# Kernel optimization log

Hardware: AMD Instinct MI355X
Metric: run time of the kernel (lower is better)

## Reference

```python
import jax, jax.numpy as jnp
import numpy as np

NUM_EMBEDDINGS = 8192
EMBEDDING_DIM = 32
L2_EPS = 1e-12  # matches torch F.normalize eps


def _l2_normalize(x, axis=-1):
    norm = jnp.linalg.norm(x, axis=axis, keepdims=True)
    return x / jnp.maximum(norm, L2_EPS)


def setup_inputs() -> dict:
    key = jax.random.key(0)
    k1, k2 = jax.random.split(key)
    inputs = jax.random.normal(k1, (32, 1024, EMBEDDING_DIM), dtype=jnp.float32)
    embeddings = jax.random.normal(k2, (NUM_EMBEDDINGS, EMBEDDING_DIM), dtype=jnp.float32)
    embeddings = _l2_normalize(embeddings, axis=1)  # buffer init: F.normalize(randn)
    return {"inputs": inputs, "embeddings": embeddings}


def reference(inputs, embeddings):
    input_shape = inputs.shape
    d = embeddings.shape[1]
    flat = inputs.reshape(-1, d)                      # [N, d]
    flat_n = _l2_normalize(flat, axis=1)              # F.normalize(flat, p=2, dim=1)
    # cosine similarity against codebook: [N, K]
    distances = jnp.einsum('nd,kd->nk', flat_n, embeddings)
    encoding_indices = jnp.argmax(distances, axis=1)  # [N]
    quantized = embeddings[encoding_indices].reshape(input_shape)
    # use_commitment=False branch: mse(quantized, inputs.detach())
    loss = jnp.mean((quantized - jax.lax.stop_gradient(inputs)) ** 2)
    # straight-through estimator
    quantized_st = inputs + jax.lax.stop_gradient(quantized - inputs)
    return quantized_st, loss, encoding_indices.reshape(input_shape[:-1])
```

## Files before the change

### kernel.cpp

```cpp
#include <hip/hip_runtime.h>

typedef short short8 __attribute__((ext_vector_type(8)));
typedef float f32x4 __attribute__((ext_vector_type(4)));

#define NROWS 32768
#define DIM 32
#define KCODES 8192
#define FLAG_CAP 4096
#define EPS_REL (1.0f/4096.0f)

#define WS_EHI  0
#define WS_ELO  (512*1024)
#define WS_IDX  (1024*1024)
#define WS_LIST (WS_IDX + 128*1024)
#define WS_CNT  (WS_LIST + FLAG_CAP*4)
#define WS_PART (WS_CNT + 64)

__device__ __forceinline__ unsigned short bf16_rne(float v){
    unsigned int u = __float_as_uint(v);
    unsigned int r = (u + 0x7fffu + ((u >> 16) & 1u)) >> 16;
    return (unsigned short)r;
}
__device__ __forceinline__ float bf16_to_f(unsigned short h){
    return __uint_as_float(((unsigned int)h) << 16);
}
__device__ __forceinline__ float dot4(const float4& a, const float4& b){
    return fmaf(a.w, b.w, fmaf(a.z, b.z, fmaf(a.y, b.y, a.x * b.x)));
}

__global__ __launch_bounds__(256) void vq_prep(
    const float* __restrict__ emb,
    unsigned short* __restrict__ ehi, unsigned short* __restrict__ elo,
    int* __restrict__ cnt)
{
    int r = blockIdx.x * 256 + threadIdx.x;
    if (r < 2) cnt[r] = 0;
    const float* er = emb + (size_t)r * DIM;
    short8* dh = (short8*)(ehi + (size_t)r * DIM);
    short8* dl = (short8*)(elo + (size_t)r * DIM);
    #pragma unroll
    for (int i = 0; i < 4; i++){
        float4 v0 = *(const float4*)(er + i*8);
        float4 v1 = *(const float4*)(er + i*8 + 4);
        float f[8] = {v0.x, v0.y, v0.z, v0.w, v1.x, v1.y, v1.z, v1.w};
        short8 a, b;
        #pragma unroll
        for (int j = 0; j < 8; j++){
            unsigned short h = bf16_rne(f[j]);
            a[j] = (short)h;
            b[j] = (short)bf16_rne(f[j] - bf16_to_f(h));
        }
        dh[i] = a; dl[i] = b;
    }
}

#define PROC(bh, bl, tcs)                                                        \
  {                                                                              \
    unsigned int tcv = (unsigned int)(tcs);                                      \
    _Pragma("unroll")                                                            \
    for (int rg = 0; rg < 4; ++rg){                                              \
      f32x4 acc = __builtin_amdgcn_mfma_f32_16x16x32_bf16(ahi[rg], bh, cbias[rg], 0, 0, 0); \
      acc = __builtin_amdgcn_mfma_f32_16x16x32_bf16(ahi[rg], bl, acc, 0, 0, 0);  \
      acc = __builtin_amdgcn_mfma_f32_16x16x32_bf16(alo[rg], bh, acc, 0, 0, 0);  \
      _Pragma("unroll")                                                          \
      for (int q = 0; q < 4; ++q){                                               \
        unsigned int u = (__float_as_uint(acc[q]) & maskv) | tcv;                \
        int rr = rg * 4 + q;                                                     \
        unsigned int nv2;                                                        \
        asm("v_med3_u32 %0, %1, %2, %3" : "=v"(nv2) : "v"(u), "v"(v1[rr]), "v"(v2[rr])); \
        v2[rr] = nv2;                                                            \
        v1[rr] = (u > v1[rr]) ? u : v1[rr];                                      \
      }                                                                          \
    }                                                                            \
  }

__global__ __launch_bounds__(512, 4) void vq_main_mfma(
    const float* __restrict__ inputs,
    const unsigned short* __restrict__ ehi,
    const unsigned short* __restrict__ elo,
    int* __restrict__ idxws, int* __restrict__ list, int* __restrict__ cnt)
{
    const int L = threadIdx.x & 63;
    const int w = threadIdx.x >> 6;
    const int rowbase = blockIdx.x * 64;

    __shared__ float snorm[64];
    __shared__ unsigned int sv1[8][64][17];
    __shared__ unsigned int sv2[8][64][17];
    __shared__ unsigned int pb1[8][64];
    __shared__ unsigned int pb2[8][64];
    __shared__ int          pbc[8][64];

    short8 ahi[4], alo[4];
    #pragma unroll
    for (int rg = 0; rg < 4; ++rg){
        const float* xr = inputs + (size_t)(rowbase + rg*16 + (L & 15)) * DIM + (L >> 4) * 8;
        float4 p0 = *(const float4*)xr;
        float4 p1 = *(const float4*)(xr + 4);
        float f[8] = {p0.x, p0.y, p0.z, p0.w, p1.x, p1.y, p1.z, p1.w};
        short8 h, l;
        #pragma unroll
        for (int i = 0; i < 8; i++){
            unsigned short hb = bf16_rne(f[i]);
            h[i] = (short)hb;
            l[i] = (short)bf16_rne(f[i] - bf16_to_f(hb));
        }
        ahi[rg] = h; alo[rg] = l;
        float s = dot4(p0, p0) + dot4(p1, p1);
        s += __shfl_xor(s, 16, 64);
        s += __shfl_xor(s, 32, 64);
        if (w == 0 && (L >> 4) == 0) snorm[rg*16 + L] = sqrtf(s);
    }
    __syncthreads();

    f32x4 cbias[4];
    #pragma unroll
    for (int rg = 0; rg < 4; ++rg){
        #pragma unroll
        for (int q = 0; q < 4; ++q)
            cbias[rg][q] = 2.0f * snorm[rg*16 + (L >> 4)*4 + q];
    }

    unsigned int maskv = 0xFFFFFFC0u;
    asm("" : "+v"(maskv));

    unsigned int v1[16], v2[16];
    #pragma unroll
    for (int r = 0; r < 16; r++){ v1[r] = 0u; v2[r] = 0u; }

    const unsigned short* ehp = ehi + (size_t)(w*1024 + (L & 15)) * DIM + (L >> 4) * 8;
    const unsigned short* elp = elo + (size_t)(w*1024 + (L & 15)) * DIM + (L >> 4) * 8;

    for (int t = 0; t < 64; t += 2){
        short8 bh0 = *(const short8*)(ehp);
        short8 bl0 = *(const short8*)(elp);
        short8 bh1 = *(const short8*)(ehp + 512);
        short8 bl1 = *(const short8*)(elp + 512);
        ehp += 1024; elp += 1024;
        PROC(bh0, bl0, 63 - t);
        PROC(bh1, bl1, 62 - t);
    }

    #pragma unroll
    for (int rg = 0; rg < 4; ++rg){
        #pragma unroll
        for (int q = 0; q < 4; ++q){
            int row = rg*16 + (L >> 4)*4 + q;
            sv1[w][row][L & 15] = v1[rg*4 + q];
            sv2[w][row][L & 15] = v2[rg*4 + q];
        }
    }
    __syncthreads();

    {
        int r = threadIdx.x & 63;
        int s = threadIdx.x >> 6;
        unsigned int b1 = 0u, b2 = 0u; int bc = 0;
        #pragma unroll
        for (int c = 0; c < 16; ++c){
            unsigned int u1 = sv1[s][r][c];
            unsigned int u2 = sv2[s][r][c];
            unsigned int mn = min(b1, u1);
            unsigned int mx = max(b2, u2);
            b2 = max(mn, mx);
            bool g = u1 > b1;
            b1 = g ? u1 : b1;
            bc = g ? c : bc;
        }
        pb1[s][r] = b1; pb2[s][r] = b2; pbc[s][r] = bc;
    }
    __syncthreads();

    if (threadIdx.x < 64){
        int r = threadIdx.x;
        unsigned int b1 = 0u, b2 = 0u; int bw = 0, bc = 0;
        #pragma unroll
        for (int s = 0; s < 8; ++s){
            unsigned int u1 = pb1[s][r];
            unsigned int u2 = pb2[s][r];
            unsigned int mn = min(b1, u1);
            unsigned int mx = max(b2, u2);
            b2 = max(mn, mx);
            bool g = u1 > b1;
            b1 = g ? u1 : b1;
            bw = g ? s : bw;
            bc = g ? pbc[s][r] : bc;
        }
        int t = 63 - (int)(b1 & 63u);
        int k = bw*1024 + t*16 + bc;
        int row = rowbase + r;
        idxws[row] = k;
        float f1 = __uint_as_float(b1 & 0xFFFFFFC0u);
        float f2 = __uint_as_float(b2 & 0xFFFFFFC0u);
        if (f1 - f2 <= snorm[r] * EPS_REL){
            int pos = atomicAdd(cnt, 1);
            if (pos < FLAG_CAP) list[pos] = row;
        }
    }
}

__global__ __launch_bounds__(256) void vq_refine(
    const float* __restrict__ inputs, const float* __restrict__ emb,
    int* __restrict__ idxws, const int* __restrict__ list, const int* __restrict__ cnt)
{
    int n = *cnt; if (n > FLAG_CAP) n = FLAG_CAP;
    __shared__ float sv[4]; __shared__ int si[4];
    for (int j = blockIdx.x; j < n; j += gridDim.x){
        int row = list[j];
        const float4* xr = (const float4*)(inputs + (size_t)row * DIM);
        float4 x0 = xr[0], x1 = xr[1], x2 = xr[2], x3 = xr[3];
        float4 x4 = xr[4], x5 = xr[5], x6 = xr[6], x7 = xr[7];
        float bv = -3.0e38f; int bi = 0x7fffffff;
        for (int c = threadIdx.x; c < KCODES; c += 256){
            const float4* ep = (const float4*)(emb + (size_t)c * DIM);
            float d = dot4(x0, ep[0]) + dot4(x1, ep[1]) + dot4(x2, ep[2]) + dot4(x3, ep[3])
                    + dot4(x4, ep[4]) + dot4(x5, ep[5]) + dot4(x6, ep[6]) + dot4(x7, ep[7]);
            if (d > bv || (d == bv && c < bi)){ bv = d; bi = c; }
        }
        #pragma unroll
        for (int off = 32; off; off >>= 1){
            float ov = __shfl_down(bv, off, 64);
            int   oi = __shfl_down(bi, off, 64);
            if (ov > bv || (ov == bv && oi < bi)){ bv = ov; bi = oi; }
        }
        if ((threadIdx.x & 63) == 0){ sv[threadIdx.x >> 6] = bv; si[threadIdx.x >> 6] = bi; }
        __syncthreads();
        if (threadIdx.x == 0){
            #pragma unroll
            for (int q = 1; q < 4; q++){
                if (sv[q] > bv || (sv[q] == bv && si[q] < bi)){ bv = sv[q]; bi = si[q]; }
            }
            idxws[row] = bi;
        }
        __syncthreads();
    }
}

__global__ __launch_bounds__(256) void vq_output(
    const float* __restrict__ inputs, const float* __restrict__ emb,
    const int* __restrict__ idxws,
    float* __restrict__ out_q, float* __restrict__ out_idx,
    float* __restrict__ part, int* __restrict__ ticket, float* __restrict__ out_loss)
{
    int row = blockIdx.x * 256 + threadIdx.x;
    int idx = idxws[row];
    const float4* ep = (const float4*)(emb + (size_t)idx * DIM);
    const float4* xr = (const float4*)(inputs + (size_t)row * DIM);
    float4* oq = (float4*)(out_q + (size_t)row * DIM);
    float s = 0.f;
    #pragma unroll
    for (int i = 0; i < 8; i++){
        float4 q = ep[i], x = xr[i];
        oq[i] = q;
        float dx = q.x - x.x, dy = q.y - x.y, dz = q.z - x.z, dw = q.w - x.w;
        s += dx*dx + dy*dy + dz*dz + dw*dw;
    }
    out_idx[row] = (float)idx;
    #pragma unroll
    for (int off = 32; off; off >>= 1) s += __shfl_down(s, off, 64);
    __shared__ float sp[4];
    __shared__ int tkt;
    if ((threadIdx.x & 63) == 0) sp[threadIdx.x >> 6] = s;
    __syncthreads();
    if (threadIdx.x == 0){
        part[blockIdx.x] = sp[0] + sp[1] + sp[2] + sp[3];
        __threadfence();
        tkt = atomicAdd(ticket, 1);
    }
    __syncthreads();
    if (tkt == (NROWS/256) - 1 && threadIdx.x < 64){
        __threadfence();
        float t = 0.f;
        for (int i = threadIdx.x; i < NROWS/256; i += 64) t += part[i];
        #pragma unroll
        for (int off = 32; off; off >>= 1) t += __shfl_down(t, off, 64);
        if (threadIdx.x == 0) *out_loss = t * (1.0f / ((float)NROWS * (float)DIM));
    }
}

extern "C" void kernel_launch(void* const* d_in, const int* in_sizes, int n_in,
                              void* d_out, int out_size, void* d_ws, size_t ws_size,
                              hipStream_t stream) {
    const float* inputs = (const float*)d_in[0];
    const float* emb    = (const float*)d_in[1];
    float* out      = (float*)d_out;
    float* out_q    = out;
    float* out_loss = out + (size_t)NROWS * DIM;
    float* out_idx  = out_loss + 1;

    char* ws = (char*)d_ws;
    unsigned short* ehi   = (unsigned short*)(ws + WS_EHI);
    unsigned short* elo   = (unsigned short*)(ws + WS_ELO);
    int*            idxws = (int*)(ws + WS_IDX);
    int*            list  = (int*)(ws + WS_LIST);
    int*            cnt   = (int*)(ws + WS_CNT);
    float*          part  = (float*)(ws + WS_PART);

    vq_prep     <<<dim3(KCODES/256), dim3(256), 0, stream>>>(emb, ehi, elo, cnt);
    vq_main_mfma<<<dim3(NROWS/64),   dim3(512), 0, stream>>>(inputs, ehi, elo, idxws, list, cnt);
    vq_refine   <<<dim3(256),        dim3(256), 0, stream>>>(inputs, emb, idxws, list, cnt);
    vq_output   <<<dim3(NROWS/256),  dim3(256), 0, stream>>>(inputs, emb, idxws, out_q, out_idx, part, cnt + 1, out_loss);
}
```

Measured before the change: 103.9 us.

## Split codebook across two blocks per row tile and fuse refine into output

The main MFMA kernel now launches twice as many blocks, each scanning half the codebook. Each block stages its top-2 candidates in the output buffer as scratch. The cross-lane reduction now uses wave shuffles and a ballot instead of a large shared-memory transpose. The separate refine kernel is removed: the output kernel merges the two halves, recomputes the input norm, flags near-ties and does the exact fp32 rescan per block before writing results. The intent is better occupancy and fewer launches and workspace round trips, at the risk of serialized per-block refine loops when many rows are flagged.

```diff
diff --git a/kernel.cpp b/kernel.cpp
--- a/kernel.cpp
+++ b/kernel.cpp
@@ -6,15 +6,12 @@
 #define NROWS 32768
 #define DIM 32
 #define KCODES 8192
-#define FLAG_CAP 4096
 #define EPS_REL (1.0f/4096.0f)
 
 #define WS_EHI  0
 #define WS_ELO  (512*1024)
-#define WS_IDX  (1024*1024)
-#define WS_LIST (WS_IDX + 128*1024)
-#define WS_CNT  (WS_LIST + FLAG_CAP*4)
-#define WS_PART (WS_CNT + 64)
+#define WS_PART (1024*1024)
+#define WS_CNT  (WS_PART + 4096)
 
 __device__ __forceinline__ unsigned short bf16_rne(float v){
     unsigned int u = __float_as_uint(v);
@@ -34,7 +31,7 @@
     int* __restrict__ cnt)
 {
     int r = blockIdx.x * 256 + threadIdx.x;
-    if (r < 2) cnt[r] = 0;
+    if (r == 0) cnt[0] = 0;
     const float* er = emb + (size_t)r * DIM;
     short8* dh = (short8*)(ehi + (size_t)r * DIM);
     short8* dl = (short8*)(elo + (size_t)r * DIM);
@@ -54,14 +51,14 @@
     }
 }
 
-#define PROC(bh, bl, tcs)                                                        \
+#define PROC(bhv, blv, tcs)                                                      \
   {                                                                              \
     unsigned int tcv = (unsigned int)(tcs);                                      \
     _Pragma("unroll")                                                            \
     for (int rg = 0; rg < 4; ++rg){                                              \
-      f32x4 acc = __builtin_amdgcn_mfma_f32_16x16x32_bf16(ahi[rg], bh, cbias[rg], 0, 0, 0); \
-      acc = __builtin_amdgcn_mfma_f32_16x16x32_bf16(ahi[rg], bl, acc, 0, 0, 0);  \
-      acc = __builtin_amdgcn_mfma_f32_16x16x32_bf16(alo[rg], bh, acc, 0, 0, 0);  \
+      f32x4 acc = __builtin_amdgcn_mfma_f32_16x16x32_bf16(ahi[rg], bhv, cbias[rg], 0, 0, 0); \
+      acc = __builtin_amdgcn_mfma_f32_16x16x32_bf16(ahi[rg], blv, acc, 0, 0, 0); \
+      acc = __builtin_amdgcn_mfma_f32_16x16x32_bf16(alo[rg], bhv, acc, 0, 0, 0); \
       _Pragma("unroll")                                                          \
       for (int q = 0; q < 4; ++q){                                               \
         unsigned int u = (__float_as_uint(acc[q]) & maskv) | tcv;                \
@@ -78,18 +75,18 @@
     const float* __restrict__ inputs,
     const unsigned short* __restrict__ ehi,
     const unsigned short* __restrict__ elo,
-    int* __restrict__ idxws, int* __restrict__ list, int* __restrict__ cnt)
+    unsigned int* __restrict__ qscr)
 {
     const int L = threadIdx.x & 63;
     const int w = threadIdx.x >> 6;
-    const int rowbase = blockIdx.x * 64;
+    const int rb    = blockIdx.x & 511;
+    const int half_ = blockIdx.x >> 9;
+    const int rowbase = rb * 64;
 
     __shared__ float snorm[64];
-    __shared__ unsigned int sv1[8][64][17];
-    __shared__ unsigned int sv2[8][64][17];
-    __shared__ unsigned int pb1[8][64];
-    __shared__ unsigned int pb2[8][64];
-    __shared__ int          pbc[8][64];
+    __shared__ unsigned int sv1[8][64];
+    __shared__ unsigned int sv2[8][64];
+    __shared__ int          scol[8][64];
 
     short8 ahi[4], alo[4];
     #pragma unroll
@@ -128,46 +125,53 @@
     #pragma unroll
     for (int r = 0; r < 16; r++){ v1[r] = 0u; v2[r] = 0u; }
 
-    const unsigned short* ehp = ehi + (size_t)(w*1024 + (L & 15)) * DIM + (L >> 4) * 8;
-    const unsigned short* elp = elo + (size_t)(w*1024 + (L & 15)) * DIM + (L >> 4) * 8;
-
-    for (int t = 0; t < 64; t += 2){
-        short8 bh0 = *(const short8*)(ehp);
-        short8 bl0 = *(const short8*)(elp);
-        short8 bh1 = *(const short8*)(ehp + 512);
-        short8 bl1 = *(const short8*)(elp + 512);
+    const int c0 = half_ * 4096 + w * 512;
+    const unsigned short* ehp = ehi + (size_t)(c0 + (L & 15)) * DIM + (L >> 4) * 8;
+    const unsigned short* elp = elo + (size_t)(c0 + (L & 15)) * DIM + (L >> 4) * 8;
+
+    for (int t = 0; t < 32; t += 2){
+        short8 b0h = *(const short8*)(ehp);
+        short8 b0l = *(const short8*)(elp);
+        short8 b1h = *(const short8*)(ehp + 512);
+        short8 b1l = *(const short8*)(elp + 512);
         ehp += 1024; elp += 1024;
-        PROC(bh0, bl0, 63 - t);
-        PROC(bh1, bl1, 62 - t);
-    }
-
-    #pragma unroll
-    for (int rg = 0; rg < 4; ++rg){
-        #pragma unroll
-        for (int q = 0; q < 4; ++q){
-            int row = rg*16 + (L >> 4)*4 + q;
-            sv1[w][row][L & 15] = v1[rg*4 + q];
-            sv2[w][row][L & 15] = v2[rg*4 + q];
-        }
-    }
-    __syncthreads();
-
-    {
-        int r = threadIdx.x & 63;
-        int s = threadIdx.x >> 6;
-        unsigned int b1 = 0u, b2 = 0u; int bc = 0;
-        #pragma unroll
-        for (int c = 0; c < 16; ++c){
-            unsigned int u1 = sv1[s][r][c];
-            unsigned int u2 = sv2[s][r][c];
-            unsigned int mn = min(b1, u1);
-            unsigned int mx = max(b2, u2);
-            b2 = max(mn, mx);
-            bool g = u1 > b1;
-            b1 = g ? u1 : b1;
-            bc = g ? c : bc;
-        }
-        pb1[s][r] = b1; pb2[s][r] = b2; pbc[s][r] = bc;
+        PROC(b0h, b0l, 31 - t);
+        PROC(b1h, b1l, 30 - t);
+    }
+
+    unsigned int p1[16];
+    #pragma unroll
+    for (int r = 0; r < 16; r++) p1[r] = v1[r];
+    #pragma unroll
+    for (int m = 1; m < 16; m <<= 1){
+        #pragma unroll
+        for (int r = 0; r < 16; r++){
+            unsigned int ov1 = __shfl_xor(v1[r], m, 64);
+            unsigned int ov2 = __shfl_xor(v2[r], m, 64);
+            unsigned int mn = min(v1[r], ov1);
+            v2[r] = max(max(v2[r], ov2), mn);
+            v1[r] = max(v1[r], ov1);
+        }
+    }
+    int colr[16];
+    #pragma unroll
+    for (int r = 0; r < 16; r++){
+        unsigned long long bm = __ballot(p1[r] == v1[r]);
+        unsigned int grp = (unsigned int)((bm >> ((L >> 4) << 4)) & 0xFFFFull);
+        colr[r] = __ffs(grp) - 1;
+    }
+
+    if ((L & 15) == 0){
+        #pragma unroll
+        for (int rg = 0; rg < 4; ++rg){
+            #pragma unroll
+            for (int q = 0; q < 4; ++q){
+                int row = rg*16 + (L >> 4)*4 + q;
+                sv1[w][row] = v1[rg*4 + q];
+                sv2[w][row] = v2[rg*4 + q];
+                scol[w][row] = colr[rg*4 + q];
+            }
+        }
     }
     __syncthreads();
 
@@ -176,45 +180,70 @@
         unsigned int b1 = 0u, b2 = 0u; int bw = 0, bc = 0;
         #pragma unroll
         for (int s = 0; s < 8; ++s){
-            unsigned int u1 = pb1[s][r];
-            unsigned int u2 = pb2[s][r];
+            unsigned int u1 = sv1[s][r];
+            unsigned int u2 = sv2[s][r];
             unsigned int mn = min(b1, u1);
-            unsigned int mx = max(b2, u2);
-            b2 = max(mn, mx);
+            b2 = max(max(b2, u2), mn);
             bool g = u1 > b1;
-            b1 = g ? u1 : b1;
-            bw = g ? s : bw;
-            bc = g ? pbc[s][r] : bc;
-        }
-        int t = 63 - (int)(b1 & 63u);
-        int k = bw*1024 + t*16 + bc;
+            if (g){ b1 = u1; bw = s; bc = scol[s][r]; }
+        }
+        int t = 31 - (int)(b1 & 63u);
+        int k = half_*4096 + bw*512 + t*16 + bc;
         int row = rowbase + r;
-        idxws[row] = k;
-        float f1 = __uint_as_float(b1 & 0xFFFFFFC0u);
-        float f2 = __uint_as_float(b2 & 0xFFFFFFC0u);
-        if (f1 - f2 <= snorm[r] * EPS_REL){
-            int pos = atomicAdd(cnt, 1);
-            if (pos < FLAG_CAP) list[pos] = row;
-        }
-    }
-}
-
-__global__ __launch_bounds__(256) void vq_refine(
+        unsigned int* qs = qscr + (size_t)row * 32 + half_ * 3;
+        qs[0] = b1; qs[1] = b2; qs[2] = (unsigned int)k;
+    }
+}
+
+__global__ __launch_bounds__(256) void vq_output(
     const float* __restrict__ inputs, const float* __restrict__ emb,
-    int* __restrict__ idxws, const int* __restrict__ list, const int* __restrict__ cnt)
+    float* __restrict__ out_q, float* __restrict__ out_idx,
+    float* __restrict__ part, int* __restrict__ ticket, float* __restrict__ out_loss)
 {
-    int n = *cnt; if (n > FLAG_CAP) n = FLAG_CAP;
+    const int row = blockIdx.x * 256 + threadIdx.x;
+    unsigned int* q32 = (unsigned int*)out_q;
+
+    unsigned int a1 = q32[(size_t)row*32 + 0];
+    unsigned int a2 = q32[(size_t)row*32 + 1];
+    unsigned int ak = q32[(size_t)row*32 + 2];
+    unsigned int b1 = q32[(size_t)row*32 + 3];
+    unsigned int b2 = q32[(size_t)row*32 + 4];
+    unsigned int bk = q32[(size_t)row*32 + 5];
+
+    unsigned int w1 = a1, wk = ak;
+    if (b1 > a1){ w1 = b1; wk = bk; }
+    unsigned int w2 = max(max(a2, b2), min(a1, b1));
+
+    const float4* xr = (const float4*)(inputs + (size_t)row * DIM);
+    float4 x0 = xr[0], x1 = xr[1], x2 = xr[2], x3 = xr[3];
+    float4 x4 = xr[4], x5 = xr[5], x6 = xr[6], x7 = xr[7];
+    float nrm = sqrtf(dot4(x0,x0)+dot4(x1,x1)+dot4(x2,x2)+dot4(x3,x3)
+                     +dot4(x4,x4)+dot4(x5,x5)+dot4(x6,x6)+dot4(x7,x7));
+
+    float f1 = __uint_as_float(w1 & 0xFFFFFFC0u);
+    float f2 = __uint_as_float(w2 & 0xFFFFFFC0u);
+    bool flag = (f1 - f2) <= nrm * EPS_REL;
+
+    __shared__ int frows[256];
+    __shared__ int corr[256];
+    __shared__ int fcnt;
+    if (threadIdx.x == 0) fcnt = 0;
+    corr[threadIdx.x] = -1;
+    __syncthreads();
+    if (flag){ int p = atomicAdd(&fcnt, 1); frows[p] = row; }
+    __syncthreads();
+
     __shared__ float sv[4]; __shared__ int si[4];
-    for (int j = blockIdx.x; j < n; j += gridDim.x){
-        int row = list[j];
-        const float4* xr = (const float4*)(inputs + (size_t)row * DIM);
-        float4 x0 = xr[0], x1 = xr[1], x2 = xr[2], x3 = xr[3];
-        float4 x4 = xr[4], x5 = xr[5], x6 = xr[6], x7 = xr[7];
+    for (int j = 0; j < fcnt; ++j){
+        int rr = frows[j];
+        const float4* yr = (const float4*)(inputs + (size_t)rr * DIM);
+        float4 y0 = yr[0], y1 = yr[1], y2 = yr[2], y3 = yr[3];
+        float4 y4 = yr[4], y5 = yr[5], y6 = yr[6], y7 = yr[7];
         float bv = -3.0e38f; int bi = 0x7fffffff;
         for (int c = threadIdx.x; c < KCODES; c += 256){
             const float4* ep = (const float4*)(emb + (size_t)c * DIM);
-            float d = dot4(x0, ep[0]) + dot4(x1, ep[1]) + dot4(x2, ep[2]) + dot4(x3, ep[3])
-                    + dot4(x4, ep[4]) + dot4(x5, ep[5]) + dot4(x6, ep[6]) + dot4(x7, ep[7]);
+            float d = dot4(y0, ep[0]) + dot4(y1, ep[1]) + dot4(y2, ep[2]) + dot4(y3, ep[3])
+                    + dot4(y4, ep[4]) + dot4(y5, ep[5]) + dot4(y6, ep[6]) + dot4(y7, ep[7]);
             if (d > bv || (d == bv && c < bi)){ bv = d; bi = c; }
         }
         #pragma unroll
@@ -230,32 +259,29 @@
             for (int q = 1; q < 4; q++){
                 if (sv[q] > bv || (sv[q] == bv && si[q] < bi)){ bv = sv[q]; bi = si[q]; }
             }
-            idxws[row] = bi;
+            corr[rr & 255] = bi;
         }
         __syncthreads();
     }
-}
-
-__global__ __launch_bounds__(256) void vq_output(
-    const float* __restrict__ inputs, const float* __restrict__ emb,
-    const int* __restrict__ idxws,
-    float* __restrict__ out_q, float* __restrict__ out_idx,
-    float* __restrict__ part, int* __restrict__ ticket, float* __restrict__ out_loss)
-{
-    int row = blockIdx.x * 256 + threadIdx.x;
-    int idx = idxws[row];
+
+    int idx = (corr[threadIdx.x] >= 0) ? corr[threadIdx.x] : (int)wk;
+
     const float4* ep = (const float4*)(emb + (size_t)idx * DIM);
-    const float4* xr = (const float4*)(inputs + (size_t)row * DIM);
     float4* oq = (float4*)(out_q + (size_t)row * DIM);
     float s = 0.f;
-    #pragma unroll
-    for (int i = 0; i < 8; i++){
-        float4 q = ep[i], x = xr[i];
-        oq[i] = q;
-        float dx = q.x - x.x, dy = q.y - x.y, dz = q.z - x.z, dw = q.w - x.w;
-        s += dx*dx + dy*dy + dz*dz + dw*dw;
+    {
+        float4 q, x;
+        q = ep[0]; x = x0; oq[0] = q; s += (q.x-x.x)*(q.x-x.x)+(q.y-x.y)*(q.y-x.y)+(q.z-x.z)*(q.z-x.z)+(q.w-x.w)*(q.w-x.w);
+        q = ep[1]; x = x1; oq[1] = q; s += (q.x-x.x)*(q.x-x.x)+(q.y-x.y)*(q.y-x.y)+(q.z-x.z)*(q.z-x.z)+(q.w-x.w)*(q.w-x.w);
+        q = ep[2]; x = x2; oq[2] = q; s += (q.x-x.x)*(q.x-x.x)+(q.y-x.y)*(q.y-x.y)+(q.z-x.z)*(q.z-x.z)+(q.w-x.w)*(q.w-x.w);
+        q = ep[3]; x = x3; oq[3] = q; s += (q.x-x.x)*(q.x-x.x)+(q.y-x.y)*(q.y-x.y)+(q.z-x.z)*(q.z-x.z)+(q.w-x.w)*(q.w-x.w);
+        q = ep[4]; x = x4; oq[4] = q; s += (q.x-x.x)*(q.x-x.x)+(q.y-x.y)*(q.y-x.y)+(q.z-x.z)*(q.z-x.z)+(q.w-x.w)*(q.w-x.w);
+        q = ep[5]; x = x5; oq[5] = q; s += (q.x-x.x)*(q.x-x.x)+(q.y-x.y)*(q.y-x.y)+(q.z-x.z)*(q.z-x.z)+(q.w-x.w)*(q.w-x.w);
+        q = ep[6]; x = x6; oq[6] = q; s += (q.x-x.x)*(q.x-x.x)+(q.y-x.y)*(q.y-x.y)+(q.z-x.z)*(q.z-x.z)+(q.w-x.w)*(q.w-x.w);
+        q = ep[7]; x = x7; oq[7] = q; s += (q.x-x.x)*(q.x-x.x)+(q.y-x.y)*(q.y-x.y)+(q.z-x.z)*(q.z-x.z)+(q.w-x.w)*(q.w-x.w);
     }
     out_idx[row] = (float)idx;
+
     #pragma unroll
     for (int off = 32; off; off >>= 1) s += __shfl_down(s, off, 64);
     __shared__ float sp[4];
@@ -289,15 +315,12 @@
     float* out_idx  = out_loss + 1;
 
     char* ws = (char*)d_ws;
-    unsigned short* ehi   = (unsigned short*)(ws + WS_EHI);
-    unsigned short* elo   = (unsigned short*)(ws + WS_ELO);
-    int*            idxws = (int*)(ws + WS_IDX);
-    int*            list  = (int*)(ws + WS_LIST);
-    int*            cnt   = (int*)(ws + WS_CNT);
-    float*          part  = (float*)(ws + WS_PART);
+    unsigned short* ehi  = (unsigned short*)(ws + WS_EHI);
+    unsigned short* elo  = (unsigned short*)(ws + WS_ELO);
+    float*          part = (float*)(ws + WS_PART);
+    int*            cnt  = (int*)(ws + WS_CNT);
 
     vq_prep     <<<dim3(KCODES/256), dim3(256), 0, stream>>>(emb, ehi, elo, cnt);
-    vq_main_mfma<<<dim3(NROWS/64),   dim3(512), 0, stream>>>(inputs, ehi, elo, idxws, list, cnt);
-    vq_refine   <<<dim3(256),        dim3(256), 0, stream>>>(inputs, emb, idxws, list, cnt);
-    vq_output   <<<dim3(NROWS/256),  dim3(256), 0, stream>>>(inputs, emb, idxws, out_q, out_idx, part, cnt + 1, out_loss);
-}
+    vq_main_mfma<<<dim3(1024),       dim3(512), 0, stream>>>(inputs, ehi, elo, (unsigned int*)out_q);
+    vq_output   <<<dim3(NROWS/256),  dim3(256), 0, stream>>>(inputs, emb, out_q, out_idx, part, cnt, out_loss);
+}
```

Result: slower. 217.3 us (+109.1%).
